# Optimization experiments

Measured on AMD Instinct MI355X. Metric: run time of the kernel, lower is better.

The kernel has to match this reference:

```python
import jax, jax.numpy as jnp
import numpy as np

B, K, DIN = 4, 512, 64
C = 64            # proj_dim
DM = 96           # d_model
NL = 3            # n_layer
PL, ST = 8, 4     # patch_len, stride
L = (K - PL) // ST + 1   # 127 patches
DI = 2 * DM              # d_inner = 192
DS = 16                  # d_state
DR = (DM + 15) // 16     # dt_rank = 6
CK = 4                   # depthwise conv kernel
PE_SCALE = 1.0


def setup_inputs() -> dict:
    key = jax.random.key(0)
    ks = jax.random.split(key, 12)
    r = lambda k, s: (0.02 * jax.random.normal(k, s)).astype(jnp.float32)
    return {
        "x": jax.random.normal(ks[0], (B, K, DIN), dtype=jnp.float32),
        "proj_w": r(ks[1], (C, DIN)), "proj_b": jnp.zeros((C,), jnp.float32),
        "embed_w": r(ks[2], (DM, PL)), "embed_b": jnp.zeros((DM,), jnp.float32),
        "pos_emb": r(ks[3], (L, DM)),
        "norm_w": jnp.ones((NL, DM), jnp.float32),
        "in_proj_w": r(ks[4], (NL, 2 * DI, DM)),
        "conv_w": r(ks[5], (NL, DI, CK)), "conv_b": jnp.zeros((NL, DI), jnp.float32),
        "x_proj_w": r(ks[6], (NL, DR + 2 * DS, DI)),
        "dt_proj_w": r(ks[7], (NL, DI, DR)),
        "dt_proj_b": jnp.full((NL, DI), -4.6, jnp.float32),
        "A_log": jnp.tile(jnp.log(jnp.arange(1, DS + 1, dtype=jnp.float32))[None, None, :], (NL, DI, 1)),
        "D": jnp.ones((NL, DI), jnp.float32),
        "out_proj_w": r(ks[8], (NL, DM, DI)),
        "norm_f_w": jnp.ones((DM,), jnp.float32),
        "fc_w": r(ks[9], (1, L * DM)), "fc_b": jnp.zeros((1,), jnp.float32),
        "head_w": r(ks[10], (2, C)), "head_b": jnp.zeros((2,), jnp.float32),
    }


def _rms(x, w, eps=1e-5):
    return x * jax.lax.rsqrt(jnp.mean(x * x, -1, keepdims=True) + eps) * w


def _causal_dwconv(x, w, b):
    # x: [N, L, DI] -> depthwise causal conv over L, kernel CK
    xt = jnp.pad(x.transpose(0, 2, 1), ((0, 0), (0, 0), (CK - 1, 0)))
    y = jax.lax.conv_general_dilated(xt, w[:, None, :], (1,), 'VALID',
                                     feature_group_count=DI,
                                     dimension_numbers=('NCH', 'OIH', 'NCH'))
    return (y + b[None, :, None]).transpose(0, 2, 1)


def _mamba_block(u, in_w, cw, cb, xp_w, dt_w, dt_b, A_log, Dp, out_w):
    # u: [N, L, DM]
    xr = jnp.einsum('nld,ed->nle', u, in_w)          # [N,L,2*DI]
    xin, res = xr[..., :DI], xr[..., DI:]
    xc = jax.nn.silu(_causal_dwconv(xin, cw, cb))    # [N,L,DI]
    dbl = jnp.einsum('nld,ed->nle', xc, xp_w)        # [N,L,DR+2*DS]
    dt, Bm, Cm = dbl[..., :DR], dbl[..., DR:DR + DS], dbl[..., DR + DS:]
    delta = jax.nn.softplus(jnp.einsum('nlr,dr->nld', dt, dt_w) + dt_b)  # [N,L,DI]
    A = -jnp.exp(A_log)                               # [DI,DS]
    dA = jnp.exp(delta[..., None] * A)                # [N,L,DI,DS]
    dBu = (delta * xc)[..., None] * Bm[:, :, None, :]

    def step(h, t):
        dA_t, dBu_t, C_t = t
        h = dA_t * h + dBu_t
        return h, jnp.einsum('nds,ns->nd', h, C_t)

    h0 = jnp.zeros((u.shape[0], DI, DS), u.dtype)
    _, ys = jax.lax.scan(step, h0, (dA.transpose(1, 0, 2, 3),
                                    dBu.transpose(1, 0, 2, 3),
                                    Cm.transpose(1, 0, 2)))
    y = ys.transpose(1, 0, 2) + xc * Dp
    y = y * jax.nn.silu(res)                          # SiLU gate (gate_off=False)
    return jnp.einsum('nld,ed->nle', y, out_w)


def reference(x, proj_w, proj_b, embed_w, embed_b, pos_emb, norm_w, in_proj_w,
              conv_w, conv_b, x_proj_w, dt_proj_w, dt_proj_b, A_log, D,
              out_proj_w, norm_f_w, fc_w, fc_b, head_w, head_b):
    # proj: permute + Conv1d 1x1 (Din -> C)
    h = jnp.einsum('bkd,cd->bck', x, proj_w) + proj_b[None, :, None]  # [B,C,K]
    # channel-independent patching
    idx = jnp.arange(L)[:, None] * ST + jnp.arange(PL)[None, :]       # [L,PL]
    patches = h[:, :, idx]                                            # [B,C,L,PL]
    e = jnp.einsum('bclp,mp->bclm', patches, embed_w) + embed_b + PE_SCALE * pos_emb
    e = e.reshape(B * C, L, DM)
    for i in range(NL):
        u = _rms(e, norm_w[i])
        e = e + _mamba_block(u, in_proj_w[i], conv_w[i], conv_b[i], x_proj_w[i],
                             dt_proj_w[i], dt_proj_b[i], A_log[i], D[i], out_proj_w[i])
    e = _rms(e, norm_f_w)
    y = e.reshape(B * C, L * DM) @ fc_w.T + fc_b      # forecast_len=1 -> [B*C,1]
    y = y.reshape(B, C)
    return jnp.einsum('bc,oc->bo', y, head_w) + head_b  # head 1x1 conv + squeeze -> [B,2]
```

## Files before the change

kernel.cpp:

```cpp
#include <hip/hip_runtime.h>
#include <math.h>

typedef __bf16 v8bf __attribute__((ext_vector_type(8)));
typedef float  v4f  __attribute__((ext_vector_type(4)));

#define NL_ 3
#define B_ 4
#define C_ 64
#define K_ 512
#define DIN_ 64
#define DM_ 96
#define L_ 127
#define PL_ 8
#define ST_ 4
#define DI_ 192
#define DS_ 16
#define DR_ 6
#define CK_ 4
#define NSEQ_ 256
#define EC_ 97
#define CH_ 32
#define XNS_ 196
#define UBS_ 104
#define CBS_ 200

#define DTT_F_CNT   (NL_*DR_*DI_)
#define WINB_B_OFF  (DTT_F_CNT*4)
#define WINB_CNT    (NL_*2*DI_*DM_)
#define WOUTB_B_OFF (WINB_B_OFF + WINB_CNT*2)
#define WOUTB_CNT   (NL_*DM_*DI_)
#define XPB_B_OFF   (WOUTB_B_OFF + WOUTB_CNT*2)
#define XPB_CNT     (NL_*(DR_+2*DS_)*DI_)
#define YV_B_OFF    (XPB_B_OFF + XPB_CNT*2)

__global__ void prep_w(const float* __restrict__ in_w,
                       const float* __restrict__ out_w,
                       const float* __restrict__ xp_w,
                       const float* __restrict__ dt_w,
                       const float* __restrict__ norm_w,
                       char* __restrict__ ws) {
  float*  dtT   = (float*)ws;
  __bf16* WinB  = (__bf16*)(ws + WINB_B_OFF);
  __bf16* WoutB = (__bf16*)(ws + WOUTB_B_OFF);
  __bf16* XpB   = (__bf16*)(ws + XPB_B_OFF);
  const int total = DTT_F_CNT + WINB_CNT + WOUTB_CNT + XPB_CNT;
  for (int idx = blockIdx.x * blockDim.x + threadIdx.x; idx < total;
       idx += gridDim.x * blockDim.x) {
    int tI = idx;
    if (tI < DTT_F_CNT) {
      int i = tI / (DR_*DI_); int rem = tI % (DR_*DI_);
      int r = rem / DI_; int d = rem % DI_;
      dtT[tI] = dt_w[(i*DI_ + d)*DR_ + r];
    } else if ((tI -= DTT_F_CNT) < WINB_CNT) {
      int i = tI / (2*DI_*DM_); int m = tI % DM_;
      WinB[tI] = (__bf16)(in_w[tI] * norm_w[i*DM_ + m]);
    } else if ((tI -= WINB_CNT) < WOUTB_CNT) {
      WoutB[tI] = (__bf16)out_w[tI];
    } else {
      tI -= WOUTB_CNT;
      XpB[tI] = (__bf16)xp_w[tI];
    }
  }
}

__global__ __launch_bounds__(512) void mamba_fused(
    const float* __restrict__ x, const float* __restrict__ proj_w,
    const float* __restrict__ proj_b, const float* __restrict__ embed_w,
    const float* __restrict__ embed_b, const float* __restrict__ pos_emb,
    const float* __restrict__ conv_w, const float* __restrict__ conv_b,
    const float* __restrict__ dt_proj_b, const float* __restrict__ Dvec,
    const float* __restrict__ norm_f_w, const float* __restrict__ fc_w,
    const float* __restrict__ fc_b, const char* __restrict__ ws,
    float* __restrict__ yout) {
  __shared__ __align__(16) float  e_s[L_*EC_];
  __shared__ __align__(16) float  xin_s[CH_*XNS_];
  __shared__ __align__(16) float  res_s[CH_*XNS_];
  __shared__ __align__(16) float  dbl_s[CH_*40];
  __shared__ __align__(16) __bf16 u_b16[CH_*UBS_];
  __shared__ __align__(16) __bf16 xc_b16[CH_*CBS_];
  __shared__ __align__(16) __bf16 y_b16[CH_*CBS_];
  __shared__ float rinv_s[128];
  __shared__ float red_s[512];

  const int n = blockIdx.x;
  const int bb = n >> 6;
  const int cc = n & 63;
  const int t = threadIdx.x;
  const int lane15 = t & 15;
  const int laneg  = (t >> 4) & 3;
  const int wv     = t >> 6;

  {
    float* const h_s  = xin_s;
    float* const ew_s = xin_s + 512;
    const float4* xr = (const float4*)(x + (size_t)(bb*K_ + t)*DIN_);
    const float4* pw = (const float4*)(proj_w + cc*DIN_);
    float acc = proj_b[cc];
#pragma unroll
    for (int j = 0; j < DIN_/4; ++j) {
      float4 a = xr[j], w = pw[j];
      acc += a.x*w.x + a.y*w.y + a.z*w.z + a.w*w.w;
    }
    h_s[t] = acc;
    for (int i = t; i < DM_*PL_; i += 512) ew_s[i] = embed_w[i];
    __syncthreads();
    for (int i = t; i < L_*DM_; i += 512) {
      int l = i / DM_, m = i - l*DM_;
      float a2 = embed_b[m] + pos_emb[i];
      const float* hp = h_s + l*ST_;
      const float* ep = ew_s + m*PL_;
#pragma unroll
      for (int p = 0; p < PL_; ++p) a2 += hp[p]*ep[p];
      e_s[l*EC_ + m] = a2;
    }
  }

  const float*  dtT_all   = (const float*)ws;
  const __bf16* WinB_all  = (const __bf16*)(ws + WINB_B_OFF);
  const __bf16* WoutB_all = (const __bf16*)(ws + WOUTB_B_OFF);
  const __bf16* XpB_all   = (const __bf16*)(ws + XPB_B_OFF);

  const int d2l = t >> 1;
  const int hf  = t & 1;

  for (int layer = 0; layer < NL_; ++layer) {
    const float* cwb  = conv_w    + layer*DI_*CK_;
    const float* cbb  = conv_b    + layer*DI_;

    v8bf Bin[3][3];
    {
      const __bf16* W = WinB_all + layer*(2*DI_*DM_);
#pragma unroll
      for (int i = 0; i < 3; ++i) {
        int e = wv*48 + i*16 + lane15;
#pragma unroll
        for (int ks = 0; ks < 3; ++ks)
          Bin[i][ks] = *(const v8bf*)(W + e*DM_ + ks*32 + laneg*8);
      }
    }
    v8bf Bout[6];
    {
      const __bf16* W = WoutB_all + layer*(DM_*DI_);
      int m = (wv < 6 ? wv : 5)*16 + lane15;
#pragma unroll
      for (int ks = 0; ks < 6; ++ks)
        Bout[ks] = *(const v8bf*)(W + m*DI_ + ks*32 + laneg*8);
    }
    v8bf Bxp[6];
    {
      const __bf16* W = XpB_all + layer*((DR_+2*DS_)*DI_);
      int ep = (wv < 3 ? wv : 0)*16 + lane15; if (ep > 37) ep = 37;
#pragma unroll
      for (int ks = 0; ks < 6; ++ks)
        Bxp[ks] = *(const v8bf*)(W + ep*DI_ + ks*32 + laneg*8);
    }

    float hreg[8], dtw[DR_];
    float dtb_r = 0.f, Dv_r = 0.f;
    float cw0=0.f, cw1=0.f, cw2=0.f, cw3=0.f, cb_r=0.f;
    float hh0=0.f, hh1=0.f, hh2=0.f;
    if (t < 2*DI_) {
      const float* dtT = dtT_all + layer*(DR_*DI_);
#pragma unroll
      for (int j = 0; j < 8; ++j) hreg[j] = 0.f;
#pragma unroll
      for (int r = 0; r < DR_; ++r) dtw[r] = dtT[r*DI_ + d2l];
      dtb_r = dt_proj_b[layer*DI_ + d2l];
      Dv_r  = Dvec[layer*DI_ + d2l];
    }
    if (t < DI_) {
      cw0 = cwb[t*CK_+0]; cw1 = cwb[t*CK_+1];
      cw2 = cwb[t*CK_+2]; cw3 = cwb[t*CK_+3];
      cb_r = cbb[t];
    }
    __syncthreads();

    for (int l0 = 0; l0 < L_; l0 += CH_) {
      const int CL = (L_ - l0 < CH_) ? (L_ - l0) : CH_;

      {
        int lrow = 4*wv + laneg;
        int lg = l0 + lrow;
        float ve[6];
        float ss = 0.f;
#pragma unroll
        for (int k = 0; k < 6; ++k) {
          float v = (lg < L_) ? e_s[lg*EC_ + lane15 + 16*k] : 0.f;
          ve[k] = v; ss += v*v;
        }
        ss += __shfl_xor(ss, 1); ss += __shfl_xor(ss, 2);
        ss += __shfl_xor(ss, 4); ss += __shfl_xor(ss, 8);
        float rv = rsqrtf(ss*(1.0f/DM_) + 1e-5f);
#pragma unroll
        for (int k = 0; k < 6; ++k)
          u_b16[lrow*UBS_ + lane15 + 16*k] =
              (lg < L_) ? (__bf16)(ve[k]*rv) : (__bf16)0.f;
      }
      __syncthreads();

#pragma unroll
      for (int lt = 0; lt < 2; ++lt) {
        const __bf16* ub = u_b16 + (lt*16 + lane15)*UBS_ + laneg*8;
        v8bf a0 = *(const v8bf*)(ub);
        v8bf a1 = *(const v8bf*)(ub + 32);
        v8bf a2 = *(const v8bf*)(ub + 64);
        v4f c0 = {0.f,0.f,0.f,0.f}, c1 = c0, c2 = c0;
        c0 = __builtin_amdgcn_mfma_f32_16x16x32_bf16(a0, Bin[0][0], c0, 0,0,0);
        c0 = __builtin_amdgcn_mfma_f32_16x16x32_bf16(a1, Bin[0][1], c0, 0,0,0);
        c0 = __builtin_amdgcn_mfma_f32_16x16x32_bf16(a2, Bin[0][2], c0, 0,0,0);
        c1 = __builtin_amdgcn_mfma_f32_16x16x32_bf16(a0, Bin[1][0], c1, 0,0,0);
        c1 = __builtin_amdgcn_mfma_f32_16x16x32_bf16(a1, Bin[1][1], c1, 0,0,0);
        c1 = __builtin_amdgcn_mfma_f32_16x16x32_bf16(a2, Bin[1][2], c1, 0,0,0);
        c2 = __builtin_amdgcn_mfma_f32_16x16x32_bf16(a0, Bin[2][0], c2, 0,0,0);
        c2 = __builtin_amdgcn_mfma_f32_16x16x32_bf16(a1, Bin[2][1], c2, 0,0,0);
        c2 = __builtin_amdgcn_mfma_f32_16x16x32_bf16(a2, Bin[2][2], c2, 0,0,0);
        int e0 = wv*48 + lane15;
        if (wv < 4) {
#pragma unroll
          for (int r = 0; r < 4; ++r) {
            int l = lt*16 + laneg*4 + r;
            xin_s[l*XNS_ + e0]      = c0[r];
            xin_s[l*XNS_ + e0 + 16] = c1[r];
            xin_s[l*XNS_ + e0 + 32] = c2[r];
          }
        } else {
          int d0 = e0 - 192;
#pragma unroll
          for (int r = 0; r < 4; ++r) {
            int l = lt*16 + laneg*4 + r;
            res_s[l*XNS_ + d0]      = c0[r];
            res_s[l*XNS_ + d0 + 16] = c1[r];
            res_s[l*XNS_ + d0 + 32] = c2[r];
          }
        }
      }
      __syncthreads();

      if (t < DI_) {
        float p0 = hh0, p1 = hh1, p2 = hh2;
        for (int l = 0; l < CL; ++l) {
          float cur = xin_s[l*XNS_ + t];
          float v = cb_r + p0*cw0 + p1*cw1 + p2*cw2 + cur*cw3;
          float sv = v / (1.f + __expf(-v));
          xc_b16[l*CBS_ + t] = (__bf16)sv;
          p0 = p1; p1 = p2; p2 = cur;
        }
        if (l0 + CH_ < L_) { hh0 = p0; hh1 = p1; hh2 = p2; }
      }
      __syncthreads();

      if (wv < 3) {
        int ep = wv*16 + lane15;
#pragma unroll
        for (int lt = 0; lt < 2; ++lt) {
          const __bf16* xb = xc_b16 + (lt*16 + lane15)*CBS_ + laneg*8;
          v8bf x0 = *(const v8bf*)(xb);
          v8bf x1 = *(const v8bf*)(xb + 32);
          v8bf x2 = *(const v8bf*)(xb + 64);
          v8bf x3 = *(const v8bf*)(xb + 96);
          v8bf x4 = *(const v8bf*)(xb + 128);
          v8bf x5 = *(const v8bf*)(xb + 160);
          v4f c = {0.f,0.f,0.f,0.f};
          c = __builtin_amdgcn_mfma_f32_16x16x32_bf16(x0, Bxp[0], c, 0,0,0);
          c = __builtin_amdgcn_mfma_f32_16x16x32_bf16(x1, Bxp[1], c, 0,0,0);
          c = __builtin_amdgcn_mfma_f32_16x16x32_bf16(x2, Bxp[2], c, 0,0,0);
          c = __builtin_amdgcn_mfma_f32_16x16x32_bf16(x3, Bxp[3], c, 0,0,0);
          c = __builtin_amdgcn_mfma_f32_16x16x32_bf16(x4, Bxp[4], c, 0,0,0);
          c = __builtin_amdgcn_mfma_f32_16x16x32_bf16(x5, Bxp[5], c, 0,0,0);
          if (ep < DR_ + 2*DS_) {
            int col = ep + (ep >= DR_ ? 2 : 0);
#pragma unroll
            for (int r = 0; r < 4; ++r)
              dbl_s[(lt*16 + laneg*4 + r)*40 + col] = c[r];
          }
        }
      }
      __syncthreads();

      if (t < 2*DI_) {
#pragma unroll 8
        for (int l = 0; l < CL; ++l) {
          const float* db = dbl_s + l*40;
          float4 dt4 = *(const float4*)(db);
          float2 dt2 = *(const float2*)(db + 4);
          float dta = dtb_r + dt4.x*dtw[0] + dt4.y*dtw[1] + dt4.z*dtw[2]
                    + dt4.w*dtw[3] + dt2.x*dtw[4] + dt2.y*dtw[5];
          float dv = (dta > 20.f) ? dta : __logf(1.f + __expf(dta));
          float xcv = (float)xc_b16[l*CBS_ + d2l];
          float du = dv * xcv;
          float rr = __expf(-dv);
          float rr2 = rr*rr, rr4 = rr2*rr2, rr8 = rr4*rr4;
          float p = hf ? rr8*rr : rr;
          const float4* bq4 = (const float4*)(db + 8 + 8*hf);
          const float4* cq4 = (const float4*)(db + 24 + 8*hf);
          float4 bA = bq4[0], bB = bq4[1], cA = cq4[0], cB = cq4[1];
          float yp = 0.f;
          hreg[0] = p*hreg[0] + du*bA.x; yp += hreg[0]*cA.x; p *= rr;
          hreg[1] = p*hreg[1] + du*bA.y; yp += hreg[1]*cA.y; p *= rr;
          hreg[2] = p*hreg[2] + du*bA.z; yp += hreg[2]*cA.z; p *= rr;
          hreg[3] = p*hreg[3] + du*bA.w; yp += hreg[3]*cA.w; p *= rr;
          hreg[4] = p*hreg[4] + du*bB.x; yp += hreg[4]*cB.x; p *= rr;
          hreg[5] = p*hreg[5] + du*bB.y; yp += hreg[5]*cB.y; p *= rr;
          hreg[6] = p*hreg[6] + du*bB.z; yp += hreg[6]*cB.z; p *= rr;
          hreg[7] = p*hreg[7] + du*bB.w; yp += hreg[7]*cB.w;
          float yo = yp + __shfl_xor(yp, 1);
          if (hf == 0) {
            float yv = yo + xcv*Dv_r;
            float r_ = res_s[l*XNS_ + d2l];
            yv *= r_ / (1.f + __expf(-r_));
            y_b16[l*CBS_ + d2l] = (__bf16)yv;
          }
        }
      }
      __syncthreads();

      if (wv < 6) {
        int m = wv*16 + lane15;
#pragma unroll
        for (int lt = 0; lt < 2; ++lt) {
          const __bf16* yb = y_b16 + (lt*16 + lane15)*CBS_ + laneg*8;
          v8bf y0 = *(const v8bf*)(yb);
          v8bf y1 = *(const v8bf*)(yb + 32);
          v8bf y2 = *(const v8bf*)(yb + 64);
          v8bf y3 = *(const v8bf*)(yb + 96);
          v8bf y4 = *(const v8bf*)(yb + 128);
          v8bf y5 = *(const v8bf*)(yb + 160);
          v4f c = {0.f,0.f,0.f,0.f};
          c = __builtin_amdgcn_mfma_f32_16x16x32_bf16(y0, Bout[0], c, 0,0,0);
          c = __builtin_amdgcn_mfma_f32_16x16x32_bf16(y1, Bout[1], c, 0,0,0);
          c = __builtin_amdgcn_mfma_f32_16x16x32_bf16(y2, Bout[2], c, 0,0,0);
          c = __builtin_amdgcn_mfma_f32_16x16x32_bf16(y3, Bout[3], c, 0,0,0);
          c = __builtin_amdgcn_mfma_f32_16x16x32_bf16(y4, Bout[4], c, 0,0,0);
          c = __builtin_amdgcn_mfma_f32_16x16x32_bf16(y5, Bout[5], c, 0,0,0);
#pragma unroll
          for (int r = 0; r < 4; ++r) {
            int l = lt*16 + laneg*4 + r;
            if (l < CL) e_s[(l0+l)*EC_ + m] += c[r];
          }
        }
      }
    }
    __syncthreads();
  }

  if (t < 508) {
    int l = t >> 2, q = t & 3;
    const float* er = e_s + l*EC_;
    float ss = 0.f;
    for (int m = q; m < DM_; m += 4) { float v = er[m]; ss += v*v; }
    ss += __shfl_xor(ss, 1); ss += __shfl_xor(ss, 2);
    if (q == 0) rinv_s[l] = rsqrtf(ss*(1.0f/DM_) + 1e-5f);
  }
  __syncthreads();
  {
    float part = 0.f;
    for (int i = t; i < L_*DM_; i += 512) {
      int l = i / DM_, m = i - l*DM_;
      part += e_s[l*EC_ + m]*rinv_s[l]*norm_f_w[m]*fc_w[i];
    }
    red_s[t] = part;
    __syncthreads();
#pragma unroll
    for (int off = 256; off > 0; off >>= 1) {
      if (t < off) red_s[t] += red_s[t + off];
      __syncthreads();
    }
    if (t == 0) yout[n] = red_s[0] + fc_b[0];
  }
}

__global__ void head_kernel(const float* __restrict__ yv,
                            const float* __restrict__ head_w,
                            const float* __restrict__ head_b,
                            float* __restrict__ out) {
  int t = threadIdx.x;
  int o = t >> 6, c = t & 63;
  for (int b = 0; b < B_; ++b) {
    float v = yv[b*C_ + c] * head_w[o*C_ + c];
    for (int off = 32; off > 0; off >>= 1) v += __shfl_down(v, off);
    if (c == 0) out[b*2 + o] = v + head_b[o];
  }
}

extern "C" void kernel_launch(void* const* d_in, const int* in_sizes, int n_in,
                              void* d_out, int out_size, void* d_ws, size_t ws_size,
                              hipStream_t stream) {
  const float* x       = (const float*)d_in[0];
  const float* proj_w  = (const float*)d_in[1];
  const float* proj_b  = (const float*)d_in[2];
  const float* embed_w = (const float*)d_in[3];
  const float* embed_b = (const float*)d_in[4];
  const float* pos_emb = (const float*)d_in[5];
  const float* norm_w  = (const float*)d_in[6];
  const float* in_w    = (const float*)d_in[7];
  const float* conv_w  = (const float*)d_in[8];
  const float* conv_b  = (const float*)d_in[9];
  const float* xp_w    = (const float*)d_in[10];
  const float* dt_w    = (const float*)d_in[11];
  const float* dt_b    = (const float*)d_in[12];
  const float* Dv      = (const float*)d_in[14];
  const float* out_w   = (const float*)d_in[15];
  const float* norm_f  = (const float*)d_in[16];
  const float* fc_w    = (const float*)d_in[17];
  const float* fc_b    = (const float*)d_in[18];
  const float* head_w  = (const float*)d_in[19];
  const float* head_b  = (const float*)d_in[20];
  char* ws   = (char*)d_ws;
  float* out = (float*)d_out;
  float* yv  = (float*)(ws + YV_B_OFF);

  const int prep_total = DTT_F_CNT + WINB_CNT + WOUTB_CNT + XPB_CNT;
  hipLaunchKernelGGL(prep_w, dim3((prep_total + 255)/256), dim3(256), 0, stream,
                     in_w, out_w, xp_w, dt_w, norm_w, ws);
  hipLaunchKernelGGL(mamba_fused, dim3(NSEQ_), dim3(512), 0, stream,
                     x, proj_w, proj_b, embed_w, embed_b, pos_emb,
                     conv_w, conv_b, dt_b, Dv, norm_f, fc_w, fc_b,
                     (const char*)ws, yv);
  hipLaunchKernelGGL(head_kernel, dim3(1), dim3(128), 0, stream,
                     yv, head_w, head_b, out);
}
```

Measured before the change: 321.0 us.

## Fuse causal depthwise conv and SiLU into in_proj MFMA epilogue via lane shuffles

Applies the causal depthwise conv and SiLU directly on the in_proj MFMA accumulators. The three previous timesteps come from neighbouring lanes via shuffles, or from carried registers across tiles and chunks. This removes the fp32 xin staging buffer, one barrier, and the serial per-channel loop over sequence positions that used only 192 threads. The gate residual is also stored as bf16 instead of fp32, which cuts shared memory but lowers precision of the gate input. Zero-padded rows in the tail chunk now feed into the carried history.

```diff
diff --git a/kernel.cpp b/kernel.cpp
--- a/kernel.cpp
+++ b/kernel.cpp
@@ -20,7 +20,6 @@
 #define NSEQ_ 256
 #define EC_ 97
 #define CH_ 32
-#define XNS_ 196
 #define UBS_ 104
 #define CBS_ 200
 
@@ -73,12 +72,11 @@
     const float* __restrict__ fc_b, const char* __restrict__ ws,
     float* __restrict__ yout) {
   __shared__ __align__(16) float  e_s[L_*EC_];
-  __shared__ __align__(16) float  xin_s[CH_*XNS_];
-  __shared__ __align__(16) float  res_s[CH_*XNS_];
   __shared__ __align__(16) float  dbl_s[CH_*40];
   __shared__ __align__(16) __bf16 u_b16[CH_*UBS_];
   __shared__ __align__(16) __bf16 xc_b16[CH_*CBS_];
   __shared__ __align__(16) __bf16 y_b16[CH_*CBS_];
+  __shared__ __align__(16) __bf16 res_b16[CH_*CBS_];
   __shared__ float rinv_s[128];
   __shared__ float red_s[512];
 
@@ -89,10 +87,11 @@
   const int lane15 = t & 15;
   const int laneg  = (t >> 4) & 3;
   const int wv     = t >> 6;
+  const int nsrc   = ((t & 63) + 48) & 63;
 
   {
-    float* const h_s  = xin_s;
-    float* const ew_s = xin_s + 512;
+    float* const h_s  = dbl_s;
+    float* const ew_s = dbl_s + 512;
     const float4* xr = (const float4*)(x + (size_t)(bb*K_ + t)*DIN_);
     const float4* pw = (const float4*)(proj_w + cc*DIN_);
     float acc = proj_b[cc];
@@ -124,9 +123,6 @@
   const int hf  = t & 1;
 
   for (int layer = 0; layer < NL_; ++layer) {
-    const float* cwb  = conv_w    + layer*DI_*CK_;
-    const float* cbb  = conv_b    + layer*DI_;
-
     v8bf Bin[3][3];
     {
       const __bf16* W = WinB_all + layer*(2*DI_*DM_);
@@ -155,10 +151,21 @@
         Bxp[ks] = *(const v8bf*)(W + ep*DI_ + ks*32 + laneg*8);
     }
 
+    const int e0 = wv*48 + lane15;
+    float cw00=0,cw01=0,cw02=0,cw03=0,cb0=0;
+    float cw10=0,cw11=0,cw12=0,cw13=0,cb1=0;
+    float cw20=0,cw21=0,cw22=0,cw23=0,cb2=0;
+    float hh00=0,hh01=0,hh02=0, hh10=0,hh11=0,hh12=0, hh20=0,hh21=0,hh22=0;
+    if (wv < 4) {
+      const float* cwb = conv_w + layer*DI_*CK_;
+      const float* cbb = conv_b + layer*DI_;
+      cw00=cwb[e0*CK_+0]; cw01=cwb[e0*CK_+1]; cw02=cwb[e0*CK_+2]; cw03=cwb[e0*CK_+3]; cb0=cbb[e0];
+      cw10=cwb[(e0+16)*CK_+0]; cw11=cwb[(e0+16)*CK_+1]; cw12=cwb[(e0+16)*CK_+2]; cw13=cwb[(e0+16)*CK_+3]; cb1=cbb[e0+16];
+      cw20=cwb[(e0+32)*CK_+0]; cw21=cwb[(e0+32)*CK_+1]; cw22=cwb[(e0+32)*CK_+2]; cw23=cwb[(e0+32)*CK_+3]; cb2=cbb[e0+32];
+    }
+
     float hreg[8], dtw[DR_];
     float dtb_r = 0.f, Dv_r = 0.f;
-    float cw0=0.f, cw1=0.f, cw2=0.f, cw3=0.f, cb_r=0.f;
-    float hh0=0.f, hh1=0.f, hh2=0.f;
     if (t < 2*DI_) {
       const float* dtT = dtT_all + layer*(DR_*DI_);
 #pragma unroll
@@ -167,11 +174,6 @@
       for (int r = 0; r < DR_; ++r) dtw[r] = dtT[r*DI_ + d2l];
       dtb_r = dt_proj_b[layer*DI_ + d2l];
       Dv_r  = Dvec[layer*DI_ + d2l];
-    }
-    if (t < DI_) {
-      cw0 = cwb[t*CK_+0]; cw1 = cwb[t*CK_+1];
-      cw2 = cwb[t*CK_+2]; cw3 = cwb[t*CK_+3];
-      cb_r = cbb[t];
     }
     __syncthreads();
 
@@ -214,38 +216,61 @@
         c2 = __builtin_amdgcn_mfma_f32_16x16x32_bf16(a0, Bin[2][0], c2, 0,0,0);
         c2 = __builtin_amdgcn_mfma_f32_16x16x32_bf16(a1, Bin[2][1], c2, 0,0,0);
         c2 = __builtin_amdgcn_mfma_f32_16x16x32_bf16(a2, Bin[2][2], c2, 0,0,0);
-        int e0 = wv*48 + lane15;
         if (wv < 4) {
+          const int lb = lt*16 + laneg*4;
+          const bool g0 = (laneg == 0);
+          {
+            float b1 = __shfl(c0[1], nsrc), b2 = __shfl(c0[2], nsrc), b3 = __shfl(c0[3], nsrc);
+            float p1 = __shfl(hh00, nsrc),  p2 = __shfl(hh01, nsrc),  p3 = __shfl(hh02, nsrc);
+            float m1 = g0 ? p1 : b1, m2 = g0 ? p2 : b2, m3 = g0 ? p3 : b3;
+            float o0 = cb0 + m1*cw00 + m2*cw01 + m3*cw02 + c0[0]*cw03;
+            float o1 = cb0 + m2*cw00 + m3*cw01 + c0[0]*cw02 + c0[1]*cw03;
+            float o2 = cb0 + m3*cw00 + c0[0]*cw01 + c0[1]*cw02 + c0[2]*cw03;
+            float o3 = cb0 + c0[0]*cw00 + c0[1]*cw01 + c0[2]*cw02 + c0[3]*cw03;
+            xc_b16[(lb+0)*CBS_ + e0] = (__bf16)(o0 / (1.f + __expf(-o0)));
+            xc_b16[(lb+1)*CBS_ + e0] = (__bf16)(o1 / (1.f + __expf(-o1)));
+            xc_b16[(lb+2)*CBS_ + e0] = (__bf16)(o2 / (1.f + __expf(-o2)));
+            xc_b16[(lb+3)*CBS_ + e0] = (__bf16)(o3 / (1.f + __expf(-o3)));
+            hh00 = c0[1]; hh01 = c0[2]; hh02 = c0[3];
+          }
+          {
+            float b1 = __shfl(c1[1], nsrc), b2 = __shfl(c1[2], nsrc), b3 = __shfl(c1[3], nsrc);
+            float p1 = __shfl(hh10, nsrc),  p2 = __shfl(hh11, nsrc),  p3 = __shfl(hh12, nsrc);
+            float m1 = g0 ? p1 : b1, m2 = g0 ? p2 : b2, m3 = g0 ? p3 : b3;
+            float o0 = cb1 + m1*cw10 + m2*cw11 + m3*cw12 + c1[0]*cw13;
+            float o1 = cb1 + m2*cw10 + m3*cw11 + c1[0]*cw12 + c1[1]*cw13;
+            float o2 = cb1 + m3*cw10 + c1[0]*cw11 + c1[1]*cw12 + c1[2]*cw13;
+            float o3 = cb1 + c1[0]*cw10 + c1[1]*cw11 + c1[2]*cw12 + c1[3]*cw13;
+            xc_b16[(lb+0)*CBS_ + e0+16] = (__bf16)(o0 / (1.f + __expf(-o0)));
+            xc_b16[(lb+1)*CBS_ + e0+16] = (__bf16)(o1 / (1.f + __expf(-o1)));
+            xc_b16[(lb+2)*CBS_ + e0+16] = (__bf16)(o2 / (1.f + __expf(-o2)));
+            xc_b16[(lb+3)*CBS_ + e0+16] = (__bf16)(o3 / (1.f + __expf(-o3)));
+            hh10 = c1[1]; hh11 = c1[2]; hh12 = c1[3];
+          }
+          {
+            float b1 = __shfl(c2[1], nsrc), b2 = __shfl(c2[2], nsrc), b3 = __shfl(c2[3], nsrc);
+            float p1 = __shfl(hh20, nsrc),  p2 = __shfl(hh21, nsrc),  p3 = __shfl(hh22, nsrc);
+            float m1 = g0 ? p1 : b1, m2 = g0 ? p2 : b2, m3 = g0 ? p3 : b3;
+            float o0 = cb2 + m1*cw20 + m2*cw21 + m3*cw22 + c2[0]*cw23;
+            float o1 = cb2 + m2*cw20 + m3*cw21 + c2[0]*cw22 + c2[1]*cw23;
+            float o2 = cb2 + m3*cw20 + c2[0]*cw21 + c2[1]*cw22 + c2[2]*cw23;
+            float o3 = cb2 + c2[0]*cw20 + c2[1]*cw21 + c2[2]*cw22 + c2[3]*cw23;
+            xc_b16[(lb+0)*CBS_ + e0+32] = (__bf16)(o0 / (1.f + __expf(-o0)));
+            xc_b16[(lb+1)*CBS_ + e0+32] = (__bf16)(o1 / (1.f + __expf(-o1)));
+            xc_b16[(lb+2)*CBS_ + e0+32] = (__bf16)(o2 / (1.f + __expf(-o2)));
+            xc_b16[(lb+3)*CBS_ + e0+32] = (__bf16)(o3 / (1.f + __expf(-o3)));
+            hh20 = c2[1]; hh21 = c2[2]; hh22 = c2[3];
+          }
+        } else {
+          const int d0 = e0 - 192;
 #pragma unroll
           for (int r = 0; r < 4; ++r) {
             int l = lt*16 + laneg*4 + r;
-            xin_s[l*XNS_ + e0]      = c0[r];
-            xin_s[l*XNS_ + e0 + 16] = c1[r];
-            xin_s[l*XNS_ + e0 + 32] = c2[r];
-          }
-        } else {
-          int d0 = e0 - 192;
-#pragma unroll
-          for (int r = 0; r < 4; ++r) {
-            int l = lt*16 + laneg*4 + r;
-            res_s[l*XNS_ + d0]      = c0[r];
-            res_s[l*XNS_ + d0 + 16] = c1[r];
-            res_s[l*XNS_ + d0 + 32] = c2[r];
+            res_b16[l*CBS_ + d0]      = (__bf16)c0[r];
+            res_b16[l*CBS_ + d0 + 16] = (__bf16)c1[r];
+            res_b16[l*CBS_ + d0 + 32] = (__bf16)c2[r];
           }
         }
-      }
-      __syncthreads();
-
-      if (t < DI_) {
-        float p0 = hh0, p1 = hh1, p2 = hh2;
-        for (int l = 0; l < CL; ++l) {
-          float cur = xin_s[l*XNS_ + t];
-          float v = cb_r + p0*cw0 + p1*cw1 + p2*cw2 + cur*cw3;
-          float sv = v / (1.f + __expf(-v));
-          xc_b16[l*CBS_ + t] = (__bf16)sv;
-          p0 = p1; p1 = p2; p2 = cur;
-        }
-        if (l0 + CH_ < L_) { hh0 = p0; hh1 = p1; hh2 = p2; }
       }
       __syncthreads();
 
@@ -306,7 +331,7 @@
           float yo = yp + __shfl_xor(yp, 1);
           if (hf == 0) {
             float yv = yo + xcv*Dv_r;
-            float r_ = res_s[l*XNS_ + d2l];
+            float r_ = (float)res_b16[l*CBS_ + d2l];
             yv *= r_ / (1.f + __expf(-r_));
             y_b16[l*CBS_ + d2l] = (__bf16)yv;
           }
```

Result: faster. 304.9 us (-5.0%).
